# Optimization experiments

Hardware: AMD Instinct MI355X
Metric: run time of the kernel (lower is better)

## Reference

```python
import jax, jax.numpy as jnp
import numpy as np
from jax import lax

B, C, T = 512, 63, 250          # batch, EEG channels, timepoints
S = 10                           # number of subjects
E = 4                            # emb_size of CNN projection
HID, PROJ = 184, 1024            # hidden_dim (=4*46), embed_dim
EPS = 1e-5
DN = ('NCHW', 'OIHW', 'NCHW')


def setup_inputs() -> dict:
    key = jax.random.key(0)
    ks = jax.random.split(key, 16)
    p = {}
    p['x'] = jax.random.normal(ks[0], (B, C, T), dtype=jnp.float32)
    p['subjects'] = jax.random.randint(ks[1], (B,), 0, S, dtype=jnp.int32)
    # per-subject Linear(T, T): weight [S, T, T], bias [S, T]
    p['W_subj'] = jax.random.normal(ks[2], (S, T, T), dtype=jnp.float32) * 0.02
    p['b_subj'] = jnp.zeros((S, T), dtype=jnp.float32)
    # tsconv
    p['conv1_w'] = jax.random.normal(ks[3], (40, 1, 1, 5), dtype=jnp.float32) * 0.1
    p['conv1_b'] = jnp.zeros((40,), dtype=jnp.float32)
    p['bn1_g'] = jnp.ones((40,), dtype=jnp.float32)
    p['bn1_b'] = jnp.zeros((40,), dtype=jnp.float32)
    p['conv2_w'] = jax.random.normal(ks[4], (40, 40, C, 1), dtype=jnp.float32) * 0.02
    p['conv2_b'] = jnp.zeros((40,), dtype=jnp.float32)
    p['bn2_g'] = jnp.ones((40,), dtype=jnp.float32)
    p['bn2_b'] = jnp.zeros((40,), dtype=jnp.float32)
    # 1x1 projection conv to emb_size
    p['proj_w'] = jax.random.normal(ks[5], (E, 40, 1, 1), dtype=jnp.float32) * 0.1
    p['proj_b'] = jnp.zeros((E,), dtype=jnp.float32)
    # MLP projector
    p['fc1_w'] = jax.random.normal(ks[6], (PROJ, HID), dtype=jnp.float32) * 0.05
    p['fc1_b'] = jnp.zeros((PROJ,), dtype=jnp.float32)
    p['fc2_w'] = jax.random.normal(ks[7], (PROJ, PROJ), dtype=jnp.float32) * 0.02
    p['fc2_b'] = jnp.zeros((PROJ,), dtype=jnp.float32)
    p['ln_g'] = jnp.ones((PROJ,), dtype=jnp.float32)
    p['ln_b'] = jnp.zeros((PROJ,), dtype=jnp.float32)
    return p


def _bn(h, g, b):
    # BatchNorm2d with batch statistics over (N, H, W), NCHW layout
    mu = jnp.mean(h, axis=(0, 2, 3), keepdims=True)
    var = jnp.var(h, axis=(0, 2, 3), keepdims=True)
    return (h - mu) * lax.rsqrt(var + EPS) * g[None, :, None, None] + b[None, :, None, None]


def _avgpool_w(h, k, s):
    # average pool over last (W) dim, kernel k stride s
    summed = lax.reduce_window(h, 0.0, lax.add, (1, 1, 1, k), (1, 1, 1, s), 'VALID')
    return summed / k


def reference(x, subjects, W_subj, b_subj, conv1_w, conv1_b, bn1_g, bn1_b,
              conv2_w, conv2_b, bn2_g, bn2_b, proj_w, proj_b,
              fc1_w, fc1_b, fc2_w, fc2_b, ln_g, ln_b):
    # --- subject-conditioned linear dispatch (grouped GEMM via gather) ---
    Wg = W_subj[subjects]                      # [B, T, T]
    bg = b_subj[subjects]                      # [B, T]
    x_eeg = jnp.einsum('bct,bst->bcs', x, Wg) + bg[:, None, :]   # [B, C, T]

    # --- Spatio_Temporal_CNN ---
    h = x_eeg[:, None, :, :]                   # [B, 1, C, T]
    h = lax.conv_general_dilated(h, conv1_w, (1, 1), 'VALID', dimension_numbers=DN)
    h = h + conv1_b[None, :, None, None]       # [B, 40, C, 246]
    h = _avgpool_w(h, 17, 5)                   # [B, 40, C, 46]
    h = jax.nn.elu(_bn(h, bn1_g, bn1_b))
    h = lax.conv_general_dilated(h, conv2_w, (1, 1), 'VALID', dimension_numbers=DN)
    h = h + conv2_b[None, :, None, None]       # [B, 40, 1, 46]
    h = jax.nn.elu(_bn(h, bn2_g, bn2_b))       # dropout = identity (eval)
    h = lax.conv_general_dilated(h, proj_w, (1, 1), 'VALID', dimension_numbers=DN)
    h = h + proj_b[None, :, None, None]        # [B, E, 1, 46]
    # Rearrange 'b e h w -> b (h w) e' then flatten -> [B, 46*E] = [B, 184]
    z = jnp.transpose(h, (0, 2, 3, 1)).reshape(h.shape[0], -1)

    # --- MLP projector ---
    h1 = z @ fc1_w.T + fc1_b                   # [B, 1024]
    r = jax.nn.gelu(h1, approximate=False) @ fc2_w.T + fc2_b
    h2 = h1 + r                                # ResidualAdd (dropout = identity)
    mu = jnp.mean(h2, axis=-1, keepdims=True)
    var = jnp.var(h2, axis=-1, keepdims=True)
    return (h2 - mu) * lax.rsqrt(var + EPS) * ln_g + ln_b
```

## Files before the change

### kernel.cpp

```cpp
#include <hip/hip_runtime.h>
#include <hip/hip_bf16.h>

#define K2 2520
#define PROJ 1024
#define HID 184
#define N1F (512.f*63.f*46.f)
#define N2F (512.f*46.f)

typedef float f32x4 __attribute__((ext_vector_type(4)));
typedef short bf16x8 __attribute__((ext_vector_type(8)));
typedef unsigned short u16;
typedef unsigned short ushort8 __attribute__((ext_vector_type(8)));

__device__ __forceinline__ u16 f2bf(float f) {
    unsigned u = __builtin_bit_cast(unsigned, f);
    return (u16)((u + 0x7FFFu + ((u >> 16) & 1u)) >> 16);
}
__device__ __forceinline__ float bf2f(u16 h) {
    unsigned u = ((unsigned)h) << 16;
    return __builtin_bit_cast(float, u);
}

__global__ void kZ(float* stats) {
    int t = threadIdx.x;
    if (t < 320) stats[t] = 0.f;
}

__global__ void kXa(const float* __restrict__ W, u16* __restrict__ Wbf) {
    int i = blockIdx.x * 256 + threadIdx.x;
    int sj = i >> 16, s_ = (i >> 8) & 255, t_ = i & 255;
    float v = (s_ < 250 && t_ < 250) ? W[(size_t)sj*62500 + s_*250 + t_] : 0.f;
    Wbf[i] = f2bf(v);
}
__global__ void kXd(const float* __restrict__ w2, u16* __restrict__ Wbf2) {
    int i = blockIdx.x * 256 + threadIdx.x;
    int n = i / 2528, k = i - n * 2528;
    float v = 0.f;
    if (n < 40 && k < K2) { int c = k / 40, o = k - c * 40; v = w2[n*K2 + o*63 + c]; }
    Wbf2[i] = f2bf(v);
}
__global__ void kXf(const float* __restrict__ fw, u16* __restrict__ fwbf1) {
    int i = blockIdx.x * 256 + threadIdx.x;
    int n = i / 192, k = i - n * 192;
    fwbf1[i] = f2bf(k < HID ? fw[n*HID + k] : 0.f);
}
__global__ void kXg(const float* __restrict__ fw, u16* __restrict__ fwbf) {
    int i = blockIdx.x * 256 + threadIdx.x;
    fwbf[i] = f2bf(fw[i]);
}

#define XS(c,s) xs[(c)*258 + (s)]
__global__ __launch_bounds__(256) void kAB(const float* __restrict__ x,
                                           const int* __restrict__ subj,
                                           const u16* __restrict__ Wbf,
                                           const float* __restrict__ bsub,
                                           const float* __restrict__ w1,
                                           const float* __restrict__ b1,
                                           u16* __restrict__ pooled,
                                           float* __restrict__ stats) {
    __shared__ float xs[64 * 258];
    __shared__ float effs[40 * 22];
    __shared__ float biasL[256];
    __shared__ float sS[6][40], sQ[6][40];
    int b = blockIdx.x;
    int sj = subj[b];
    int tid = threadIdx.x;

    biasL[tid] = (tid < 250) ? bsub[sj*250 + tid] : 0.f;
    for (int i = tid; i < 840; i += 256) {
        int o = i / 21, j = i - o * 21;
        float e = 0.f;
        #pragma unroll
        for (int k = 0; k < 5; ++k) { int u = j - k; if (u >= 0 && u <= 16) e += w1[o*5 + k]; }
        effs[o*22 + j] = e * (1.f / 17.f);
    }

    int wv = tid >> 6, lane = tid & 63, row = lane & 15, kg = lane >> 4;
    int c = wv*16 + row;
    const float* xr = x + ((size_t)b*63 + (c < 63 ? c : 62))*250;
    const u16* Wb = Wbf + (size_t)sj*65536;
    f32x4 acc[16];
    #pragma unroll
    for (int i = 0; i < 16; ++i) acc[i] = (f32x4){0.f,0.f,0.f,0.f};

    #pragma unroll
    for (int ks = 0; ks < 8; ++ks) {
        int tb = ks*32 + kg*8;
        float av[8];
        if (ks < 7) {
            #pragma unroll
            for (int j = 0; j < 8; j += 2) { float2 v = *(const float2*)&xr[tb+j]; av[j]=v.x; av[j+1]=v.y; }
        } else {
            #pragma unroll
            for (int j = 0; j < 8; ++j) av[j] = 0.f;
            if (kg < 3) {
                #pragma unroll
                for (int j = 0; j < 8; j += 2) { float2 v = *(const float2*)&xr[tb+j]; av[j]=v.x; av[j+1]=v.y; }
            } else {
                float2 v = *(const float2*)&xr[248]; av[0]=v.x; av[1]=v.y;
            }
        }
        bf16x8 af;
        #pragma unroll
        for (int j = 0; j < 8; ++j) af[j] = (short)f2bf(av[j]);
        #pragma unroll
        for (int nf = 0; nf < 16; ++nf) {
            bf16x8 bv = *(const bf16x8*)(Wb + (size_t)(nf*16 + row)*256 + tb);
            acc[nf] = __builtin_amdgcn_mfma_f32_16x16x32_bf16(af, bv, acc[nf], 0, 0, 0);
        }
    }
    __syncthreads();
    int cD = wv*16 + kg*4;
    #pragma unroll
    for (int nf = 0; nf < 16; ++nf) {
        int s = nf*16 + row;
        float bias = biasL[s];
        #pragma unroll
        for (int r = 0; r < 4; ++r) XS(cD + r, s) = acc[nf][r] + bias;
    }
    __syncthreads();

    float ssum = 0.f, ssq = 0.f;
    if (tid < 240) {
        int o = tid % 40, cg = tid / 40;
        float eff[21];
        #pragma unroll
        for (int j = 0; j < 21; ++j) eff[j] = effs[o*22 + j];
        float bo = b1[o];
        u16* prow = pooled + (size_t)b * 46 * K2;
        for (int c2 = cg; c2 < 63; c2 += 6) {
            float win[21];
            #pragma unroll
            for (int j = 0; j < 21; ++j) win[j] = XS(c2, j);
            int kidx = c2*40 + o;
            #pragma unroll
            for (int w = 0; w < 46; ++w) {
                float a = bo;
                #pragma unroll
                for (int j = 0; j < 21; ++j) a = fmaf(win[j], eff[j], a);
                prow[(size_t)w*K2 + kidx] = f2bf(a);
                ssum += a; ssq += a*a;
                if (w < 45) {
                    #pragma unroll
                    for (int j2 = 0; j2 < 16; ++j2) win[j2] = win[j2+5];
                    #pragma unroll
                    for (int j2 = 16; j2 < 21; ++j2) win[j2] = XS(c2, 5*w + 5 + j2);
                }
            }
        }
        sS[cg][o] = ssum; sQ[cg][o] = ssq;
    }
    __syncthreads();
    if (tid < 40) {
        float s = 0.f, q = 0.f;
        #pragma unroll
        for (int g = 0; g < 6; ++g) { s += sS[g][tid]; q += sQ[g][tid]; }
        atomicAdd(&stats[tid], s);
        atomicAdd(&stats[40 + tid], q);
    }
}

__global__ void kC(float* stats, const float* __restrict__ g1, const float* __restrict__ bb1) {
    int t = threadIdx.x;
    if (t < 40) {
        float mean = stats[t] / N1F;
        float var  = stats[40 + t] / N1F - mean * mean;
        float sc   = g1[t] * rsqrtf(var + 1e-5f);
        stats[80 + t]  = sc;
        stats[120 + t] = bb1[t] - mean * sc;
    }
}

__global__ __launch_bounds__(256) void kD(const u16* __restrict__ pooled,
                                          const u16* __restrict__ Wbf2,
                                          const float* __restrict__ b2,
                                          const float* __restrict__ stats,
                                          float* __restrict__ out2,
                                          float* __restrict__ statw) {
    __shared__ float2 scsh[40];
    __shared__ float mrg[2][64][12];
    __shared__ float redS[2][48], redQ[2][48];
    int tid = threadIdx.x;
    if (tid < 40) scsh[tid] = make_float2(stats[80 + tid], stats[120 + tid]);
    __syncthreads();
    int wv = tid >> 6, lane = tid & 63, row = lane & 15, kg = lane >> 4;
    int rowgrp = wv >> 1, khalf = wv & 1;
    int mbase = blockIdx.x*32 + rowgrp*16;
    const u16* pr = pooled + (size_t)(mbase + row) * K2;
    f32x4 acc[3];
    #pragma unroll
    for (int i = 0; i < 3; ++i) acc[i] = (f32x4){0.f,0.f,0.f,0.f};

    int ksBeg = khalf ? 39 : 0, ksEnd = khalf ? 79 : 39;
    for (int ks = ksBeg; ks < ksEnd; ++ks) {
        int kbase = ks*32 + kg*8;
        ushort8 cur = *(const ushort8*)&pr[kbase];
        bf16x8 bv0 = *(const bf16x8*)(Wbf2 + (size_t)(row     )*2528 + kbase);
        bf16x8 bv1 = *(const bf16x8*)(Wbf2 + (size_t)(16 + row)*2528 + kbase);
        bf16x8 bv2 = *(const bf16x8*)(Wbf2 + (size_t)(32 + row)*2528 + kbase);
        bf16x8 af;
        bool valid = (ks < 78) | (kg < 3);
        if (valid) {
            #pragma unroll
            for (int j = 0; j < 8; ++j) {
                int k = kbase + j;
                int u = (k * 1639) >> 16;
                int o = k - u*40;
                float2 ss = scsh[o];
                float a = fmaf(bf2f(cur[j]), ss.x, ss.y);
                float e = a > 0.f ? a : __expf(a) - 1.f;
                af[j] = (short)f2bf(e);
            }
        } else {
            #pragma unroll
            for (int j = 0; j < 8; ++j) af[j] = 0;
        }
        acc[0] = __builtin_amdgcn_mfma_f32_16x16x32_bf16(af, bv0, acc[0], 0, 0, 0);
        acc[1] = __builtin_amdgcn_mfma_f32_16x16x32_bf16(af, bv1, acc[1], 0, 0, 0);
        acc[2] = __builtin_amdgcn_mfma_f32_16x16x32_bf16(af, bv2, acc[2], 0, 0, 0);
    }

    if (khalf) {
        #pragma unroll
        for (int nf = 0; nf < 3; ++nf)
            #pragma unroll
            for (int r = 0; r < 4; ++r) mrg[rowgrp][lane][nf*4 + r] = acc[nf][r];
    }
    __syncthreads();
    if (!khalf) {
        float sN[3] = {0.f,0.f,0.f}, qN[3] = {0.f,0.f,0.f};
        #pragma unroll
        for (int nf = 0; nf < 3; ++nf) {
            int n = nf*16 + row;
            #pragma unroll
            for (int r = 0; r < 4; ++r) acc[nf][r] += mrg[rowgrp][lane][nf*4 + r];
            if (n < 40) {
                float bias = b2[n];
                #pragma unroll
                for (int r = 0; r < 4; ++r) {
                    float v = acc[nf][r] + bias;
                    out2[(size_t)(mbase + kg*4 + r)*40 + n] = v;
                    sN[nf] += v; qN[nf] += v*v;
                }
            }
        }
        #pragma unroll
        for (int nf = 0; nf < 3; ++nf) {
            float s = sN[nf], q = qN[nf];
            s += __shfl_xor(s, 16); q += __shfl_xor(q, 16);
            s += __shfl_xor(s, 32); q += __shfl_xor(q, 32);
            if (kg == 0) { redS[rowgrp][nf*16 + row] = s; redQ[rowgrp][nf*16 + row] = q; }
        }
    }
    __syncthreads();
    if (tid < 40) {
        atomicAdd(&statw[160 + tid], redS[0][tid] + redS[1][tid]);
        atomicAdd(&statw[200 + tid], redQ[0][tid] + redQ[1][tid]);
    }
}

__global__ void kE2(float* stats, const float* __restrict__ g2, const float* __restrict__ bb2) {
    int t = threadIdx.x;
    if (t < 40) {
        float mean = stats[160 + t] / N2F;
        float var  = stats[200 + t] / N2F - mean * mean;
        float s    = g2[t] * rsqrtf(var + 1e-5f);
        stats[240 + t] = s;
        stats[280 + t] = bb2[t] - mean * s;
    }
}

__global__ void kF(const float* __restrict__ out2, const float* __restrict__ stats,
                   const float* __restrict__ pw, const float* __restrict__ pb,
                   u16* __restrict__ zbf) {
    int b = blockIdx.x, t = threadIdx.x;
    __shared__ float sc[40], sh[40], pws[160];
    __shared__ float o2[1840];
    if (t < 40) { sc[t] = stats[240 + t]; sh[t] = stats[280 + t]; }
    if (t < 160) pws[t] = pw[t];
    for (int i = t; i < 1840; i += 256) o2[i] = out2[(size_t)b*1840 + i];
    __syncthreads();
    if (t < 192) {
        float accv = 0.f;
        if (t < HID) {
            int w = t >> 2, e = t & 3;
            accv = pb[e];
            for (int o = 0; o < 40; ++o) {
                float a = o2[w*40 + o];
                float act = a * sc[o] + sh[o];
                act = act > 0.f ? act : __expf(act) - 1.f;
                accv = fmaf(act, pws[e*40 + o], accv);
            }
        }
        zbf[(size_t)b*192 + t] = f2bf(accv);
    }
}

__global__ __launch_bounds__(256) void kG1(const u16* __restrict__ zbf, const u16* __restrict__ fwbf1,
                                           const float* __restrict__ fb,
                                           float* __restrict__ h1, u16* __restrict__ gbf) {
    int n0 = blockIdx.x * 64, m0 = blockIdx.y * 16;
    int tid = threadIdx.x, wv = tid >> 6, lane = tid & 63, row = lane & 15, kg = lane >> 4;
    const u16* zr = zbf + (size_t)(m0 + row) * 192;
    const u16* wr = fwbf1 + (size_t)(n0 + wv*16 + row) * 192;
    f32x4 acc = (f32x4){0.f,0.f,0.f,0.f};
    #pragma unroll
    for (int ks = 0; ks < 6; ++ks) {
        bf16x8 av = *(const bf16x8*)(zr + ks*32 + kg*8);
        bf16x8 bv = *(const bf16x8*)(wr + ks*32 + kg*8);
        acc = __builtin_amdgcn_mfma_f32_16x16x32_bf16(av, bv, acc, 0, 0, 0);
    }
    int n = n0 + wv*16 + row;
    float bias = fb[n];
    #pragma unroll
    for (int r = 0; r < 4; ++r) {
        int m = m0 + kg*4 + r;
        float v = acc[r] + bias;
        h1[(size_t)m*PROJ + n] = v;
        float ge = 0.5f * v * (1.f + erff(v * 0.70710678118f));
        gbf[(size_t)m*PROJ + n] = f2bf(ge);
    }
}

__global__ __launch_bounds__(256) void kG2(const u16* __restrict__ gbf, const u16* __restrict__ fwbf,
                                           const float* __restrict__ fb, const float* __restrict__ h1,
                                           float* __restrict__ h2) {
    int n0 = blockIdx.x * 32, m0 = blockIdx.y * 64;
    int tid = threadIdx.x;
    int wv = tid >> 6, lane = tid & 63, row = lane & 15, kg = lane >> 4;
    const u16* gr = gbf + (size_t)(m0 + wv*16 + row) * PROJ;
    f32x4 acc[2];
    #pragma unroll
    for (int i = 0; i < 2; ++i) acc[i] = (f32x4){0.f,0.f,0.f,0.f};
    for (int ks = 0; ks < 32; ++ks) {
        int kbase = ks*32 + kg*8;
        bf16x8 av  = *(const bf16x8*)(gr + kbase);
        bf16x8 bv0 = *(const bf16x8*)(fwbf + (size_t)(n0      + row)*PROJ + kbase);
        bf16x8 bv1 = *(const bf16x8*)(fwbf + (size_t)(n0 + 16 + row)*PROJ + kbase);
        acc[0] = __builtin_amdgcn_mfma_f32_16x16x32_bf16(av, bv0, acc[0], 0, 0, 0);
        acc[1] = __builtin_amdgcn_mfma_f32_16x16x32_bf16(av, bv1, acc[1], 0, 0, 0);
    }
    int m = m0 + wv*16 + kg*4;
    #pragma unroll
    for (int nf = 0; nf < 2; ++nf) {
        int n = n0 + nf*16 + row;
        float bias = fb[n];
        #pragma unroll
        for (int r = 0; r < 4; ++r)
            h2[(size_t)(m + r)*PROJ + n] = acc[nf][r] + bias + h1[(size_t)(m + r)*PROJ + n];
    }
}

__global__ __launch_bounds__(256) void kG3(const float* __restrict__ h2, const float* __restrict__ lg,
                                           const float* __restrict__ lb, float* __restrict__ out) {
    int b = blockIdx.x, tid = threadIdx.x;
    float4 v = *(const float4*)&h2[(size_t)b*PROJ + tid*4];
    float s = v.x + v.y + v.z + v.w;
    float q = v.x*v.x + v.y*v.y + v.z*v.z + v.w*v.w;
    __shared__ float ps[4], pq[4], mb[2];
    int wave = tid >> 6, lane = tid & 63;
    #pragma unroll
    for (int d = 32; d >= 1; d >>= 1) { s += __shfl_down(s, d); q += __shfl_down(q, d); }
    if (lane == 0) { ps[wave] = s; pq[wave] = q; }
    __syncthreads();
    if (tid == 0) {
        float S = ps[0]+ps[1]+ps[2]+ps[3], Q = pq[0]+pq[1]+pq[2]+pq[3];
        float mean = S / 1024.f, var = Q / 1024.f - mean*mean;
        mb[0] = mean; mb[1] = rsqrtf(var + 1e-5f);
    }
    __syncthreads();
    float mean = mb[0], inv = mb[1];
    float4 g4 = *(const float4*)&lg[tid*4];
    float4 b4 = *(const float4*)&lb[tid*4];
    float4 o4;
    o4.x = (v.x - mean)*inv*g4.x + b4.x;
    o4.y = (v.y - mean)*inv*g4.y + b4.y;
    o4.z = (v.z - mean)*inv*g4.z + b4.z;
    o4.w = (v.w - mean)*inv*g4.w + b4.w;
    *(float4*)&out[(size_t)b*PROJ + tid*4] = o4;
}

extern "C" void kernel_launch(void* const* d_in, const int* in_sizes, int n_in,
                              void* d_out, int out_size, void* d_ws, size_t ws_size,
                              hipStream_t stream) {
    const float* x       = (const float*)d_in[0];
    const int*   subjects= (const int*)  d_in[1];
    const float* W_subj  = (const float*)d_in[2];
    const float* b_subj  = (const float*)d_in[3];
    const float* conv1_w = (const float*)d_in[4];
    const float* conv1_b = (const float*)d_in[5];
    const float* bn1_g   = (const float*)d_in[6];
    const float* bn1_b   = (const float*)d_in[7];
    const float* conv2_w = (const float*)d_in[8];
    const float* conv2_b = (const float*)d_in[9];
    const float* bn2_g   = (const float*)d_in[10];
    const float* bn2_b   = (const float*)d_in[11];
    const float* proj_w  = (const float*)d_in[12];
    const float* proj_b  = (const float*)d_in[13];
    const float* fc1_w   = (const float*)d_in[14];
    const float* fc1_b   = (const float*)d_in[15];
    const float* fc2_w   = (const float*)d_in[16];
    const float* fc2_b   = (const float*)d_in[17];
    const float* ln_g    = (const float*)d_in[18];
    const float* ln_b    = (const float*)d_in[19];
    float* out = (float*)d_out;

    char* ws = (char*)d_ws;
    u16*   pooled = (u16*)  ws;
    float* out2   = (float*)(ws + 118702144);
    u16*   zbf    = (u16*)  (ws + 122470464);
    float* h1     = (float*)(ws + 122667072);
    float* h2     = (float*)(ws + 124764224);
    u16*   gbf    = (u16*)  (ws + 126861376);
    float* stats  = (float*)(ws + 127909952);
    u16*   Wbf    = (u16*)  (ws + 127914048);
    u16*   Wbf2   = (u16*)  (ws + 129224768);
    u16*   fwbf2  = (u16*)  (ws + 129467456);
    u16*   fwbf1  = (u16*)  (ws + 131564608);

    kZ  <<<1, 512, 0, stream>>>(stats);
    kXa <<<2560, 256, 0, stream>>>(W_subj, Wbf);
    kXd <<<474, 256, 0, stream>>>(conv2_w, Wbf2);
    kXf <<<768, 256, 0, stream>>>(fc1_w, fwbf1);
    kXg <<<4096, 256, 0, stream>>>(fc2_w, fwbf2);
    kAB <<<512, 256, 0, stream>>>(x, subjects, Wbf, b_subj, conv1_w, conv1_b, pooled, stats);
    kC  <<<1, 64, 0, stream>>>(stats, bn1_g, bn1_b);
    kD  <<<736, 256, 0, stream>>>(pooled, Wbf2, conv2_b, stats, out2, stats);
    kE2 <<<1, 64, 0, stream>>>(stats, bn2_g, bn2_b);
    kF  <<<512, 256, 0, stream>>>(out2, stats, proj_w, proj_b, zbf);
    kG1 <<<dim3(16, 32), 256, 0, stream>>>(zbf, fwbf1, fc1_b, h1, gbf);
    kG2 <<<dim3(32, 8), 256, 0, stream>>>(gbf, fwbf2, fc2_b, h1, h2);
    kG3 <<<512, 256, 0, stream>>>(h2, ln_g, ln_b, out);
    (void)in_sizes; (void)n_in; (void)out_size; (void)ws_size;
}
```

Measured before the change: 291.0 us.

## Merge weight-conversion kernels and split kAB across two channel halves

The five small setup kernels (zeroing stats plus four weight-to-bf16 conversions) are merged into one launch with block-index ranges, which removes launch overhead. kAB now runs on a 512x2 grid, with each block handling 32 channels. Its four waves are split as 2 channel groups by 2 halves of the output columns, which halves shared memory and the accumulator registers so more blocks can be resident. The cost is that the x rows and the bias/filter setup are loaded redundantly by each half.

```diff
diff --git a/kernel.cpp b/kernel.cpp
--- a/kernel.cpp
+++ b/kernel.cpp
@@ -21,32 +21,31 @@
     return __builtin_bit_cast(float, u);
 }
 
-__global__ void kZ(float* stats) {
-    int t = threadIdx.x;
-    if (t < 320) stats[t] = 0.f;
-}
-
-__global__ void kXa(const float* __restrict__ W, u16* __restrict__ Wbf) {
-    int i = blockIdx.x * 256 + threadIdx.x;
-    int sj = i >> 16, s_ = (i >> 8) & 255, t_ = i & 255;
-    float v = (s_ < 250 && t_ < 250) ? W[(size_t)sj*62500 + s_*250 + t_] : 0.f;
-    Wbf[i] = f2bf(v);
-}
-__global__ void kXd(const float* __restrict__ w2, u16* __restrict__ Wbf2) {
-    int i = blockIdx.x * 256 + threadIdx.x;
-    int n = i / 2528, k = i - n * 2528;
-    float v = 0.f;
-    if (n < 40 && k < K2) { int c = k / 40, o = k - c * 40; v = w2[n*K2 + o*63 + c]; }
-    Wbf2[i] = f2bf(v);
-}
-__global__ void kXf(const float* __restrict__ fw, u16* __restrict__ fwbf1) {
-    int i = blockIdx.x * 256 + threadIdx.x;
-    int n = i / 192, k = i - n * 192;
-    fwbf1[i] = f2bf(k < HID ? fw[n*HID + k] : 0.f);
-}
-__global__ void kXg(const float* __restrict__ fw, u16* __restrict__ fwbf) {
-    int i = blockIdx.x * 256 + threadIdx.x;
-    fwbf[i] = f2bf(fw[i]);
+__global__ void kX(const float* __restrict__ W, const float* __restrict__ w2,
+                   const float* __restrict__ fw1, const float* __restrict__ fw2,
+                   u16* __restrict__ Wbf, u16* __restrict__ Wbf2,
+                   u16* __restrict__ fwbf1, u16* __restrict__ fwbf2, float* stats) {
+    int bid = blockIdx.x, tid = threadIdx.x;
+    if (bid == 0 && tid < 320) stats[tid] = 0.f;
+    if (bid < 2560) {
+        int i = bid*256 + tid;
+        int sj = i >> 16, s_ = (i >> 8) & 255, t_ = i & 255;
+        float v = (s_ < 250 && t_ < 250) ? W[(size_t)sj*62500 + s_*250 + t_] : 0.f;
+        Wbf[i] = f2bf(v);
+    } else if (bid < 3034) {
+        int i = (bid-2560)*256 + tid;
+        int n = i / 2528, k = i - n*2528;
+        float v = 0.f;
+        if (n < 40 && k < K2) { int c = k/40, o = k - c*40; v = w2[n*K2 + o*63 + c]; }
+        Wbf2[i] = f2bf(v);
+    } else if (bid < 3802) {
+        int i = (bid-3034)*256 + tid;
+        int n = i/192, k = i - n*192;
+        fwbf1[i] = f2bf(k < HID ? fw1[n*HID + k] : 0.f);
+    } else {
+        int i = (bid-3802)*256 + tid;
+        fwbf2[i] = f2bf(fw2[i]);
+    }
 }
 
 #define XS(c,s) xs[(c)*258 + (s)]
@@ -58,31 +57,31 @@
                                            const float* __restrict__ b1,
                                            u16* __restrict__ pooled,
                                            float* __restrict__ stats) {
-    __shared__ float xs[64 * 258];
+    __shared__ float xs[32 * 258];
     __shared__ float effs[40 * 22];
     __shared__ float biasL[256];
     __shared__ float sS[6][40], sQ[6][40];
-    int b = blockIdx.x;
+    int b = blockIdx.x, ch = blockIdx.y;
     int sj = subj[b];
     int tid = threadIdx.x;
+    int wv = tid >> 6, lane = tid & 63, row = lane & 15, kg = lane >> 4;
 
     biasL[tid] = (tid < 250) ? bsub[sj*250 + tid] : 0.f;
     for (int i = tid; i < 840; i += 256) {
         int o = i / 21, j = i - o * 21;
         float e = 0.f;
         #pragma unroll
-        for (int k = 0; k < 5; ++k) { int u = j - k; if (u >= 0 && u <= 16) e += w1[o*5 + k]; }
+        for (int k = 0; k < 5; ++k) { int u = j - k; if (u >= 0 && u <= 16) e += w1[o*5+k]; }
         effs[o*22 + j] = e * (1.f / 17.f);
     }
 
-    int wv = tid >> 6, lane = tid & 63, row = lane & 15, kg = lane >> 4;
-    int c = wv*16 + row;
-    const float* xr = x + ((size_t)b*63 + (c < 63 ? c : 62))*250;
+    int cgrp = wv & 1, nfh = wv >> 1;
+    int cglob = ch*32 + cgrp*16 + row;
+    const float* xr = x + ((size_t)b*63 + (cglob < 63 ? cglob : 62))*250;
     const u16* Wb = Wbf + (size_t)sj*65536;
-    f32x4 acc[16];
-    #pragma unroll
-    for (int i = 0; i < 16; ++i) acc[i] = (f32x4){0.f,0.f,0.f,0.f};
-
+    f32x4 acc[8];
+    #pragma unroll
+    for (int i = 0; i < 8; ++i) acc[i] = (f32x4){0.f,0.f,0.f,0.f};
     #pragma unroll
     for (int ks = 0; ks < 8; ++ks) {
         int tb = ks*32 + kg*8;
@@ -104,42 +103,44 @@
         #pragma unroll
         for (int j = 0; j < 8; ++j) af[j] = (short)f2bf(av[j]);
         #pragma unroll
-        for (int nf = 0; nf < 16; ++nf) {
+        for (int nf2 = 0; nf2 < 8; ++nf2) {
+            int nf = nfh*8 + nf2;
             bf16x8 bv = *(const bf16x8*)(Wb + (size_t)(nf*16 + row)*256 + tb);
-            acc[nf] = __builtin_amdgcn_mfma_f32_16x16x32_bf16(af, bv, acc[nf], 0, 0, 0);
-        }
-    }
-    __syncthreads();
-    int cD = wv*16 + kg*4;
-    #pragma unroll
-    for (int nf = 0; nf < 16; ++nf) {
-        int s = nf*16 + row;
+            acc[nf2] = __builtin_amdgcn_mfma_f32_16x16x32_bf16(af, bv, acc[nf2], 0, 0, 0);
+        }
+    }
+    __syncthreads();
+    int cw = cgrp*16 + kg*4;
+    #pragma unroll
+    for (int nf2 = 0; nf2 < 8; ++nf2) {
+        int s = (nfh*8 + nf2)*16 + row;
         float bias = biasL[s];
         #pragma unroll
-        for (int r = 0; r < 4; ++r) XS(cD + r, s) = acc[nf][r] + bias;
-    }
-    __syncthreads();
-
-    float ssum = 0.f, ssq = 0.f;
+        for (int r = 0; r < 4; ++r) XS(cw + r, s) = acc[nf2][r] + bias;
+    }
+    __syncthreads();
+
+    int climit = ch ? 31 : 32;
     if (tid < 240) {
         int o = tid % 40, cg = tid / 40;
         float eff[21];
         #pragma unroll
         for (int j = 0; j < 21; ++j) eff[j] = effs[o*22 + j];
         float bo = b1[o];
+        float ssum = 0.f, ssq = 0.f;
         u16* prow = pooled + (size_t)b * 46 * K2;
-        for (int c2 = cg; c2 < 63; c2 += 6) {
+        for (int c2 = cg; c2 < climit; c2 += 6) {
             float win[21];
             #pragma unroll
             for (int j = 0; j < 21; ++j) win[j] = XS(c2, j);
-            int kidx = c2*40 + o;
+            int kidx = (ch*32 + c2)*40 + o;
             #pragma unroll
             for (int w = 0; w < 46; ++w) {
                 float a = bo;
                 #pragma unroll
                 for (int j = 0; j < 21; ++j) a = fmaf(win[j], eff[j], a);
                 prow[(size_t)w*K2 + kidx] = f2bf(a);
-                ssum += a; ssq += a*a;
+                ssum += a; ssq = fmaf(a, a, ssq);
                 if (w < 45) {
                     #pragma unroll
                     for (int j2 = 0; j2 < 16; ++j2) win[j2] = win[j2+5];
@@ -206,8 +207,8 @@
                 int k = kbase + j;
                 int u = (k * 1639) >> 16;
                 int o = k - u*40;
-                float2 ss = scsh[o];
-                float a = fmaf(bf2f(cur[j]), ss.x, ss.y);
+                float2 sshf = scsh[o];
+                float a = fmaf(bf2f(cur[j]), sshf.x, sshf.y);
                 float e = a > 0.f ? a : __expf(a) - 1.f;
                 af[j] = (short)f2bf(e);
             }
@@ -418,12 +419,8 @@
     u16*   fwbf2  = (u16*)  (ws + 129467456);
     u16*   fwbf1  = (u16*)  (ws + 131564608);
 
-    kZ  <<<1, 512, 0, stream>>>(stats);
-    kXa <<<2560, 256, 0, stream>>>(W_subj, Wbf);
-    kXd <<<474, 256, 0, stream>>>(conv2_w, Wbf2);
-    kXf <<<768, 256, 0, stream>>>(fc1_w, fwbf1);
-    kXg <<<4096, 256, 0, stream>>>(fc2_w, fwbf2);
-    kAB <<<512, 256, 0, stream>>>(x, subjects, Wbf, b_subj, conv1_w, conv1_b, pooled, stats);
+    kX  <<<7898, 256, 0, stream>>>(W_subj, conv2_w, fc1_w, fc2_w, Wbf, Wbf2, fwbf1, fwbf2, stats);
+    kAB <<<dim3(512, 2), 256, 0, stream>>>(x, subjects, Wbf, b_subj, conv1_w, conv1_b, pooled, stats);
     kC  <<<1, 64, 0, stream>>>(stats, bn1_g, bn1_b);
     kD  <<<736, 256, 0, stream>>>(pooled, Wbf2, conv2_b, stats, out2, stats);
     kE2 <<<1, 64, 0, stream>>>(stats, bn2_g, bn2_b);
```

Result: no change. 291.4 us (+0.1%).
